# Kernel optimization log

Measured on AMD Instinct MI355X. Metric: run time of the kernel, lower is better.

## Reference

```python
import jax, jax.numpy as jnp
import numpy as np

BASE_SCALE = 60.0
EPS = 1e-8


def _nearest_D8(x):
    """Nearest point in D8 lattice (integer vectors with even coordinate sum), x: [..., 8]."""
    f = jnp.round(x)
    d = x - f
    parity_even = (jnp.mod(jnp.sum(f, axis=-1), 2.0) == 0.0)
    # flip rounding at the coordinate with the largest rounding error
    idx = jnp.argmax(jnp.abs(d), axis=-1)
    delta = jnp.where(d >= 0, 1.0, -1.0).astype(x.dtype)
    onehot = jax.nn.one_hot(idx, 8, dtype=x.dtype)
    flip = jnp.take_along_axis(delta, idx[..., None], axis=-1)
    g = f + onehot * flip
    return jnp.where(parity_even[..., None], f, g)


def _e8_quantize(x):
    """Nearest point in E8 = D8 U (D8 + 1/2), x: [..., 8]."""
    y0 = _nearest_D8(x)
    y1 = _nearest_D8(x - 0.5) + 0.5
    d0 = jnp.sum((x - y0) ** 2, axis=-1, keepdims=True)
    d1 = jnp.sum((x - y1) ** 2, axis=-1, keepdims=True)
    return jnp.where(d0 <= d1, y0, y1)


def _quantize_with_row_scaling(w):
    """Row-norm scale -> E8 lattice quantize on 8-dim blocks -> rescale back."""
    n_rows = w.shape[0]
    adaptive = min(2.0, max(0.5, n_rows / 10000.0))
    sf = jnp.asarray(BASE_SCALE * adaptive, dtype=w.dtype)
    row_norms = jnp.linalg.norm(w, axis=1, keepdims=True)  # [out, 1]
    row_norms_safe = jnp.maximum(row_norms, EPS)
    w_scaled = (w / row_norms_safe) * sf
    q = _e8_quantize(w_scaled.reshape(-1, 8)).reshape(w.shape)
    return q * row_norms_safe / sf


def setup_inputs() -> dict:
    key = jax.random.key(0)
    k1, k2, k3 = jax.random.split(key, 3)
    B, IN, OUT = 4096, 4096, 4096
    x = jax.random.normal(k1, (B, IN), dtype=jnp.float32)
    weight = jax.random.normal(k2, (OUT, IN), dtype=jnp.float32) * 0.1
    bias = jax.random.normal(k3, (OUT,), dtype=jnp.float32)
    return {"x": x, "weight": weight, "bias": bias}


def reference(x, weight, bias):
    wq = _quantize_with_row_scaling(weight)
    return x @ wq.T + bias
```

## Files before the change

### kernel.cpp

```cpp
#include <hip/hip_runtime.h>
#include <hip/hip_bf16.h>

typedef __bf16 bf16_t;
typedef __bf16 bf16x8 __attribute__((ext_vector_type(8)));
typedef float f32x4 __attribute__((ext_vector_type(4)));

#define GLL16(gp, lp)                                                          \
    __builtin_amdgcn_global_load_lds(                                          \
        (const __attribute__((address_space(1))) void*)(gp),                   \
        (__attribute__((address_space(3))) void*)(lp), 16, 0, 0)

#define SBAR() __builtin_amdgcn_s_barrier()
#define SCHED0() __builtin_amdgcn_sched_barrier(0)
#define WAIT_VM8() asm volatile("s_waitcnt vmcnt(8)" ::: "memory")
#define WAIT_VM0() asm volatile("s_waitcnt vmcnt(0)" ::: "memory")
#define WAIT_LGKM0() asm volatile("s_waitcnt lgkmcnt(0)" ::: "memory")
#define MFMA_(d, a, b)                                                         \
    d = __builtin_amdgcn_mfma_f32_16x16x32_bf16(a, b, d, 0, 0, 0)


__device__ __forceinline__ void nearest_D8_d(const double x[8], double f[8]) {
    double d[8];
    double fs = 0.0;
#pragma unroll
    for (int i = 0; i < 8; ++i) {
        f[i] = rint(x[i]);
        d[i] = x[i] - f[i];
        fs += f[i];
    }
    long long s = (long long)fs;
    if (s & 1LL) {
        int idx = 0;
        double best = fabs(d[0]);
#pragma unroll
        for (int i = 1; i < 8; ++i) {
            double a = fabs(d[i]);
            if (a > best) { best = a; idx = i; }
        }
        f[idx] += (d[idx] >= 0.0) ? 1.0 : -1.0;
    }
}

__device__ __forceinline__ void e8_quantize_d(const double x[8], float q[8]) {
    double y0[8], y1[8], xs[8];
    nearest_D8_d(x, y0);
#pragma unroll
    for (int i = 0; i < 8; ++i) xs[i] = x[i] - 0.5;
    nearest_D8_d(xs, y1);
#pragma unroll
    for (int i = 0; i < 8; ++i) y1[i] += 0.5;
    double d0 = 0.0, d1 = 0.0;
#pragma unroll
    for (int i = 0; i < 8; ++i) {
        double a = x[i] - y0[i]; d0 += a * a;
        double b = x[i] - y1[i]; d1 += b * b;
    }
    bool take0 = (d0 <= d1);
#pragma unroll
    for (int i = 0; i < 8; ++i) q[i] = (float)(take0 ? y0[i] : y1[i]);
}

__global__ __launch_bounds__(256) void prep_kernel(
    const float* __restrict__ W, bf16_t* __restrict__ Q,
    float* __restrict__ scale, int IN, double sfd,
    const float* __restrict__ x, bf16_t* __restrict__ Xb, long long n8,
    int OUT, int CB)
{
    if (blockIdx.x >= (unsigned)OUT) {
        long long i = (long long)(blockIdx.x - OUT) * 256 + threadIdx.x;
        long long stride = (long long)CB * 256;
        for (; i < n8; i += stride) {
            float4 v0 = *(const float4*)(x + i * 8);
            float4 v1 = *(const float4*)(x + i * 8 + 4);
            bf16x8 o;
            o[0] = (bf16_t)v0.x; o[1] = (bf16_t)v0.y;
            o[2] = (bf16_t)v0.z; o[3] = (bf16_t)v0.w;
            o[4] = (bf16_t)v1.x; o[5] = (bf16_t)v1.y;
            o[6] = (bf16_t)v1.z; o[7] = (bf16_t)v1.w;
            *(bf16x8*)(Xb + i * 8) = o;
        }
        return;
    }
    const int row  = blockIdx.x;
    const int t    = threadIdx.x;
    const int lane = t & 63, w = t >> 6;
    const float* wrow = W + (size_t)row * IN;

    double ss = 0.0;
    for (int i = t; i < (IN >> 2); i += 256) {
        float4 v = *(const float4*)(wrow + i * 4);
        double a = v.x, b = v.y, c = v.z, d = v.w;
        ss += a * a + b * b + c * c + d * d;
    }
#pragma unroll
    for (int m = 1; m < 64; m <<= 1) ss += __shfl_xor(ss, m);
    __shared__ double red[4];
    if (lane == 0) red[w] = ss;
    __syncthreads();
    double S   = (red[0] + red[1]) + (red[2] + red[3]);
    double nsd = fmax(sqrt(S), 1e-8);

    for (int b = t; b < (IN >> 3); b += 256) {
        const float* xp = wrow + b * 8;
        float4 v0 = *(const float4*)xp;
        float4 v1 = *(const float4*)(xp + 4);
        double xd[8] = {v0.x, v0.y, v0.z, v0.w, v1.x, v1.y, v1.z, v1.w};
        double xsd[8];
#pragma unroll
        for (int i = 0; i < 8; ++i) xsd[i] = (xd[i] / nsd) * sfd;
        float qf[8];
        e8_quantize_d(xsd, qf);
        bf16x8 o;
#pragma unroll
        for (int i = 0; i < 8; ++i) o[i] = (bf16_t)qf[i];
        *(bf16x8*)(Q + (size_t)row * IN + b * 8) = o;
    }
    if (t == 0) scale[row] = (float)(nsd / sfd);
}


#define BM 256
#define BN 256
#define BK 64

__global__ __launch_bounds__(512, 2) void gemm_kernel(
    const bf16_t* __restrict__ A,
    const bf16_t* __restrict__ B,
    const float* __restrict__ scale,
    const float* __restrict__ bias,
    float* __restrict__ C,
    int M, int N, int K)
{
    __shared__ __align__(16) bf16_t lds[2][2][2][8192];

    const int t    = threadIdx.x;
    const int lane = t & 63;
    const int w    = t >> 6;
    const int wr   = w >> 2;
    const int wc   = w & 3;

    const int nwg = gridDim.x;
    const int bid = blockIdx.x;
    const int q8 = nwg >> 3, r8 = nwg & 7;
    const int xcd = bid & 7, idx = bid >> 3;
    const int swz = (xcd < r8 ? xcd * (q8 + 1) : r8 * (q8 + 1) + (xcd - r8) * q8) + idx;
    const int nbx = N / BN;
    const int bx = swz % nbx, by = swz / nbx;

    const int rowq  = t >> 3;
    const int kslot = ((t & 7) ^ (rowq & 7)) << 3;
    const bf16_t* gA = A + (size_t)(by * BM + rowq) * K + kslot;
    const bf16_t* gB = B + (size_t)(bx * BN + rowq) * K + kslot;

#define STAGE(isB, bufi, h, kt)                                                \
    do {                                                                       \
        const bf16_t* s_ = ((isB) ? gB : gA)                                   \
            + (size_t)(h) * 128 * (size_t)K + (size_t)(kt) * BK;               \
        GLL16(s_,                   &lds[bufi][isB][h][t * 8]);                \
        GLL16(s_ + 64 * (size_t)K,  &lds[bufi][isB][h][t * 8 + 4096]);         \
    } while (0)

    const int l15  = lane & 15;
    const int koff = lane >> 4;
    const int aoff0 = l15 * 64 + (((koff)     ^ (lane & 7)) << 3);
    const int aoff1 = l15 * 64 + (((4 + koff) ^ (lane & 7)) << 3);

    f32x4 acc[8][4];
    const f32x4 zero = {0.f, 0.f, 0.f, 0.f};
#pragma unroll
    for (int R = 0; R < 8; ++R)
#pragma unroll
        for (int Cf = 0; Cf < 4; ++Cf) acc[R][Cf] = zero;

    const int NT = K / BK;

    STAGE(1, 0, 0, 0); STAGE(1, 0, 1, 0);
    STAGE(0, 0, 0, 0); STAGE(0, 0, 1, 0);
    STAGE(1, 1, 0, 1); STAGE(1, 1, 1, 1);
    STAGE(0, 1, 0, 1); STAGE(0, 1, 1, 1);
    WAIT_VM8();
    SBAR();
    SCHED0();

    bf16x8 fA0[8], fA1[8], fB0[4], fB1[4];

    {
        const bf16_t* ldsA0 = &lds[0][0][wr][0];
        const bf16_t* ldsB0 = &lds[0][1][wc >> 1][(wc & 1) * 4096];
#pragma unroll
        for (int R = 0; R < 8; ++R)
            fA0[R] = *(const bf16x8*)(ldsA0 + R * 1024 + aoff0);
#pragma unroll
        for (int c = 0; c < 4; ++c)
            fB0[c] = *(const bf16x8*)(ldsB0 + c * 1024 + aoff0);
    }

    for (int kt = 0; kt < NT; ++kt) {
        const int cur = kt & 1;
        const bf16_t* ldsAc = &lds[cur][0][wr][0];
        const bf16_t* ldsBc = &lds[cur][1][wc >> 1][(wc & 1) * 4096];
        const bf16_t* ldsAn = &lds[cur ^ 1][0][wr][0];
        const bf16_t* ldsBn = &lds[cur ^ 1][1][wc >> 1][(wc & 1) * 4096];

#pragma unroll
        for (int R = 0; R < 8; ++R)
            fA1[R] = *(const bf16x8*)(ldsAc + R * 1024 + aoff1);
#pragma unroll
        for (int c = 0; c < 4; ++c)
            fB1[c] = *(const bf16x8*)(ldsBc + c * 1024 + aoff1);
        __builtin_amdgcn_s_setprio(1);
#pragma unroll
        for (int R = 0; R < 8; ++R)
#pragma unroll
            for (int c = 0; c < 4; ++c)
                MFMA_(acc[R][c], fA0[R], fB0[c]);
        __builtin_amdgcn_s_setprio(0);
        SCHED0();
        WAIT_LGKM0();
        SBAR();
        SCHED0();

        if (kt + 2 < NT) {
            STAGE(1, cur, 0, kt + 2); STAGE(1, cur, 1, kt + 2);
            STAGE(0, cur, 0, kt + 2); STAGE(0, cur, 1, kt + 2);
        }
        __builtin_amdgcn_s_setprio(1);
#pragma unroll
        for (int R = 0; R < 8; ++R) {
            MFMA_(acc[R][0], fA1[R], fB1[0]);
            MFMA_(acc[R][1], fA1[R], fB1[1]);
        }
        __builtin_amdgcn_s_setprio(0);
        SCHED0();
        if (kt < NT - 2) { WAIT_VM8(); }
        else if (kt == NT - 2) { WAIT_VM0(); }
        SBAR();
        SCHED0();

        if (kt + 1 < NT) {
#pragma unroll
            for (int R = 0; R < 8; ++R)
                fA0[R] = *(const bf16x8*)(ldsAn + R * 1024 + aoff0);
#pragma unroll
            for (int c = 0; c < 4; ++c)
                fB0[c] = *(const bf16x8*)(ldsBn + c * 1024 + aoff0);
        }
        __builtin_amdgcn_s_setprio(1);
#pragma unroll
        for (int R = 0; R < 8; ++R) {
            MFMA_(acc[R][2], fA1[R], fB1[2]);
            MFMA_(acc[R][3], fA1[R], fB1[3]);
        }
        __builtin_amdgcn_s_setprio(0);
    }

    const int r0 = by * BM + wr * 128 + (lane >> 4) * 4;
    const int c0 = bx * BN + wc * 64 + l15;
#pragma unroll
    for (int Cf = 0; Cf < 4; ++Cf) {
        const int col = c0 + Cf * 16;
        const float sc = scale[col];
        const float bi = bias[col];
#pragma unroll
        for (int R = 0; R < 8; ++R) {
            const int row = r0 + R * 16;
#pragma unroll
            for (int j = 0; j < 4; ++j)
                C[(size_t)(row + j) * N + col] = acc[R][Cf][j] * sc + bi;
        }
    }
#undef STAGE
}


extern "C" void kernel_launch(void* const* d_in, const int* in_sizes, int n_in,
                              void* d_out, int out_size, void* d_ws, size_t ws_size,
                              hipStream_t stream)
{
    const float* x    = (const float*)d_in[0];
    const float* wgt  = (const float*)d_in[1];
    const float* bias = (const float*)d_in[2];

    const int OUT = in_sizes[2];
    const int IN  = (int)((long long)in_sizes[1] / OUT);
    const int M   = (int)((long long)in_sizes[0] / IN);
    const int N = OUT, K = IN;

    double ad = (double)OUT / 10000.0;
    if (ad < 0.5) ad = 0.5;
    if (ad > 2.0) ad = 2.0;
    const double sfd = 60.0 * ad;

    bf16_t* Q  = (bf16_t*)d_ws;
    bf16_t* Xb = (bf16_t*)((char*)d_ws + (size_t)OUT * IN * sizeof(bf16_t));
    float*  sc = (float*)((char*)d_ws + (size_t)OUT * IN * sizeof(bf16_t)
                                      + (size_t)M * IN * sizeof(bf16_t));
    float*  C  = (float*)d_out;

    long long n8 = (long long)M * IN / 8;
    const int CB = 2048;
    prep_kernel<<<OUT + CB, 256, 0, stream>>>(wgt, Q, sc, IN, sfd,
                                              x, Xb, n8, OUT, CB);

    int grid = (M / BM) * (N / BN);
    gemm_kernel<<<grid, 512, 0, stream>>>(Xb, Q, sc, bias, C, M, N, K);
}
```

Before: 158.2 us.

## Restructure GEMM main loop into 8-phase quadrant schedule with interleaved staging

Replaces the two-half K-step loop with an unrolled two-K-tile iteration that splits each tile into four quadrant MFMA phases. Each phase issues a smaller LDS fragment read and one global-to-LDS stage, separated by barriers and finer waitcnts. Register fragments shrink from full 8x4 A/B sets to 4x2 quadrant sets. The goal is to overlap global loads, LDS reads and MFMAs more evenly and lower register pressure, at the cost of more barriers per K-tile and an assumption that NT is even.

Result: no change. 158.4 us (median of 3 runs) (+0.2%).

```diff
diff --git a/kernel.cpp b/kernel.cpp
--- a/kernel.cpp
+++ b/kernel.cpp
@@ -12,8 +12,9 @@
 
 #define SBAR() __builtin_amdgcn_s_barrier()
 #define SCHED0() __builtin_amdgcn_sched_barrier(0)
-#define WAIT_VM8() asm volatile("s_waitcnt vmcnt(8)" ::: "memory")
+#define WAIT_VM4() asm volatile("s_waitcnt vmcnt(4)" ::: "memory")
 #define WAIT_VM0() asm volatile("s_waitcnt vmcnt(0)" ::: "memory")
+#define WAIT_LGKM8() asm volatile("s_waitcnt lgkmcnt(8)" ::: "memory")
 #define WAIT_LGKM0() asm volatile("s_waitcnt lgkmcnt(0)" ::: "memory")
 #define MFMA_(d, a, b)                                                         \
     d = __builtin_amdgcn_mfma_f32_16x16x32_bf16(a, b, d, 0, 0, 0)
@@ -173,85 +174,108 @@
         for (int Cf = 0; Cf < 4; ++Cf) acc[R][Cf] = zero;
 
     const int NT = K / BK;
-
+    const int NI = NT / 2;
+
+    const bf16_t* A0p = &lds[0][0][wr][0];
+    const bf16_t* B0p = &lds[0][1][wc >> 1][(wc & 1) * 4096];
+    const bf16_t* A1p = &lds[1][0][wr][0];
+    const bf16_t* B1p = &lds[1][1][wc >> 1][(wc & 1) * 4096];
+
+    bf16x8 af[4][2], b01[2][2], b23[2][2];
+
+#define RD_A03(AP)                                                             \
+    _Pragma("unroll")                                                          \
+    for (int R = 0; R < 4; ++R) {                                              \
+        af[R][0] = *(const bf16x8*)((AP) + R * 1024 + aoff0);                  \
+        af[R][1] = *(const bf16x8*)((AP) + R * 1024 + aoff1);                  \
+    }
+#define RD_A47(AP)                                                             \
+    _Pragma("unroll")                                                          \
+    for (int R = 0; R < 4; ++R) {                                              \
+        af[R][0] = *(const bf16x8*)((AP) + (4 + R) * 1024 + aoff0);            \
+        af[R][1] = *(const bf16x8*)((AP) + (4 + R) * 1024 + aoff1);            \
+    }
+#define RD_B01(BP)                                                             \
+    _Pragma("unroll")                                                          \
+    for (int c = 0; c < 2; ++c) {                                              \
+        b01[c][0] = *(const bf16x8*)((BP) + c * 1024 + aoff0);                 \
+        b01[c][1] = *(const bf16x8*)((BP) + c * 1024 + aoff1);                 \
+    }
+#define RD_B23(BP)                                                             \
+    _Pragma("unroll")                                                          \
+    for (int c = 0; c < 2; ++c) {                                              \
+        b23[c][0] = *(const bf16x8*)((BP) + (2 + c) * 1024 + aoff0);           \
+        b23[c][1] = *(const bf16x8*)((BP) + (2 + c) * 1024 + aoff1);           \
+    }
+#define PH_MID() do { SBAR(); WAIT_LGKM0(); SCHED0();                          \
+                      __builtin_amdgcn_s_setprio(1); } while (0)
+#define PH_END() do { __builtin_amdgcn_s_setprio(0); SBAR(); } while (0)
+#define MM_Q(RB, CB, AF, BF)                                                   \
+    _Pragma("unroll")                                                          \
+    for (int s = 0; s < 2; ++s)                                                \
+        _Pragma("unroll")                                                      \
+        for (int R = 0; R < 4; ++R) {                                          \
+            MFMA_(acc[(RB) + R][(CB)],     AF[R][s], BF[0][s]);                \
+            MFMA_(acc[(RB) + R][(CB) + 1], AF[R][s], BF[1][s]);                \
+        }
+
+    STAGE(0, 0, 0, 0); STAGE(0, 0, 1, 0);
     STAGE(1, 0, 0, 0); STAGE(1, 0, 1, 0);
-    STAGE(0, 0, 0, 0); STAGE(0, 0, 1, 0);
     STAGE(1, 1, 0, 1); STAGE(1, 1, 1, 1);
-    STAGE(0, 1, 0, 1); STAGE(0, 1, 1, 1);
-    WAIT_VM8();
+    WAIT_VM4();
     SBAR();
     SCHED0();
 
-    bf16x8 fA0[8], fA1[8], fB0[4], fB1[4];
+    for (int i = 0; i < NI - 1; ++i) {
+        const int E = 2 * i;
+        RD_A03(A0p); RD_B01(B0p);
+        STAGE(0, 1, 0, E + 1);
+        WAIT_LGKM8();
+        PH_MID(); MM_Q(0, 0, af, b01); PH_END();
+        RD_B23(B0p);
+        STAGE(0, 1, 1, E + 1);
+        PH_MID(); MM_Q(0, 2, af, b23); PH_END();
+        RD_A47(A0p);
+        STAGE(1, 0, 0, E + 2);
+        PH_MID(); MM_Q(4, 2, af, b23); PH_END();
+        STAGE(1, 0, 1, E + 2);
+        WAIT_VM4();
+        PH_MID(); MM_Q(4, 0, af, b01); PH_END();
+        RD_A03(A1p); RD_B01(B1p);
+        STAGE(0, 0, 0, E + 2);
+        WAIT_LGKM8();
+        PH_MID(); MM_Q(0, 0, af, b01); PH_END();
+        RD_B23(B1p);
+        STAGE(0, 0, 1, E + 2);
+        PH_MID(); MM_Q(0, 2, af, b23); PH_END();
+        RD_A47(A1p);
+        STAGE(1, 1, 0, E + 3);
+        PH_MID(); MM_Q(4, 2, af, b23); PH_END();
+        STAGE(1, 1, 1, E + 3);
+        WAIT_VM4();
+        PH_MID(); MM_Q(4, 0, af, b01); PH_END();
+    }
 
     {
-        const bf16_t* ldsA0 = &lds[0][0][wr][0];
-        const bf16_t* ldsB0 = &lds[0][1][wc >> 1][(wc & 1) * 4096];
-#pragma unroll
-        for (int R = 0; R < 8; ++R)
-            fA0[R] = *(const bf16x8*)(ldsA0 + R * 1024 + aoff0);
-#pragma unroll
-        for (int c = 0; c < 4; ++c)
-            fB0[c] = *(const bf16x8*)(ldsB0 + c * 1024 + aoff0);
-    }
-
-    for (int kt = 0; kt < NT; ++kt) {
-        const int cur = kt & 1;
-        const bf16_t* ldsAc = &lds[cur][0][wr][0];
-        const bf16_t* ldsBc = &lds[cur][1][wc >> 1][(wc & 1) * 4096];
-        const bf16_t* ldsAn = &lds[cur ^ 1][0][wr][0];
-        const bf16_t* ldsBn = &lds[cur ^ 1][1][wc >> 1][(wc & 1) * 4096];
-
-#pragma unroll
-        for (int R = 0; R < 8; ++R)
-            fA1[R] = *(const bf16x8*)(ldsAc + R * 1024 + aoff1);
-#pragma unroll
-        for (int c = 0; c < 4; ++c)
-            fB1[c] = *(const bf16x8*)(ldsBc + c * 1024 + aoff1);
-        __builtin_amdgcn_s_setprio(1);
-#pragma unroll
-        for (int R = 0; R < 8; ++R)
-#pragma unroll
-            for (int c = 0; c < 4; ++c)
-                MFMA_(acc[R][c], fA0[R], fB0[c]);
-        __builtin_amdgcn_s_setprio(0);
-        SCHED0();
-        WAIT_LGKM0();
-        SBAR();
-        SCHED0();
-
-        if (kt + 2 < NT) {
-            STAGE(1, cur, 0, kt + 2); STAGE(1, cur, 1, kt + 2);
-            STAGE(0, cur, 0, kt + 2); STAGE(0, cur, 1, kt + 2);
-        }
-        __builtin_amdgcn_s_setprio(1);
-#pragma unroll
-        for (int R = 0; R < 8; ++R) {
-            MFMA_(acc[R][0], fA1[R], fB1[0]);
-            MFMA_(acc[R][1], fA1[R], fB1[1]);
-        }
-        __builtin_amdgcn_s_setprio(0);
-        SCHED0();
-        if (kt < NT - 2) { WAIT_VM8(); }
-        else if (kt == NT - 2) { WAIT_VM0(); }
-        SBAR();
-        SCHED0();
-
-        if (kt + 1 < NT) {
-#pragma unroll
-            for (int R = 0; R < 8; ++R)
-                fA0[R] = *(const bf16x8*)(ldsAn + R * 1024 + aoff0);
-#pragma unroll
-            for (int c = 0; c < 4; ++c)
-                fB0[c] = *(const bf16x8*)(ldsBn + c * 1024 + aoff0);
-        }
-        __builtin_amdgcn_s_setprio(1);
-#pragma unroll
-        for (int R = 0; R < 8; ++R) {
-            MFMA_(acc[R][2], fA1[R], fB1[2]);
-            MFMA_(acc[R][3], fA1[R], fB1[3]);
-        }
-        __builtin_amdgcn_s_setprio(0);
+        RD_A03(A0p); RD_B01(B0p);
+        STAGE(0, 1, 0, NT - 1);
+        WAIT_LGKM8();
+        PH_MID(); MM_Q(0, 0, af, b01); PH_END();
+        RD_B23(B0p);
+        STAGE(0, 1, 1, NT - 1);
+        PH_MID(); MM_Q(0, 2, af, b23); PH_END();
+        RD_A47(A0p);
+        PH_MID(); MM_Q(4, 2, af, b23); PH_END();
+        WAIT_VM0();
+        PH_MID(); MM_Q(4, 0, af, b01); PH_END();
+        RD_A03(A1p); RD_B01(B1p);
+        WAIT_LGKM8();
+        PH_MID(); MM_Q(0, 0, af, b01); PH_END();
+        RD_B23(B1p);
+        PH_MID(); MM_Q(0, 2, af, b23); PH_END();
+        RD_A47(A1p);
+        PH_MID(); MM_Q(4, 2, af, b23); PH_END();
+        PH_MID(); MM_Q(4, 0, af, b01); PH_END();
     }
 
     const int r0 = by * BM + wr * 128 + (lane >> 4) * 4;
@@ -270,6 +294,13 @@
         }
     }
 #undef STAGE
+#undef RD_A03
+#undef RD_A47
+#undef RD_B01
+#undef RD_B23
+#undef PH_MID
+#undef PH_END
+#undef MM_Q
 }
 
 
```
